# Kernel optimization log

Hardware: AMD Instinct MI355X
Metric: run time of the kernel (lower is better)

## Reference

```python
import jax, jax.numpy as jnp
import numpy as np

B, I, O, ORDER = 16384, 256, 256, 8
LO, HI = -1.0, 1.0


def setup_inputs() -> dict:
    key = jax.random.key(0)
    k1, k2, k3 = jax.random.split(key, 3)
    x = jax.random.normal(k1, (B, I), dtype=jnp.float32)
    weights = jax.random.normal(k2, (O, I), dtype=jnp.float32)
    # BernsteinBasisFunction init: randn(order+1) * 0.1, one per (o, i) pair
    coeffs = jax.random.normal(k3, (O, I, ORDER + 1), dtype=jnp.float32) * 0.1
    return {"x": x, "weights": weights, "coeffs": coeffs}


def reference(x, weights, coeffs):
    # x: [B, I]; weights: [O, I]; coeffs: [O, I, K+1]
    K = coeffs.shape[-1] - 1
    zoom = (HI - LO) / 2.0
    pan = (HI + LO) / 2.0
    xt = jnp.tanh(x) * zoom + pan          # squash into [LO, HI]
    x_a = xt - LO                          # [B, I]
    x_b = HI - xt                          # [B, I]
    e = jnp.arange(K + 1)
    # ber[b, i, k] = x_a^k * x_b^(K-k)  (unnormalized Bernstein basis)
    ber = (x_a[..., None] ** e) * (x_b[..., None] ** (K - e))  # [B, I, K+1]
    # transformed[b, o, i] = sum_k coeffs[o,i,k] * ber[b,i,k]; out = einsum('boi,oi->bo')
    # Fused: fold weights into coeffs to avoid the [B, O, I] intermediate.
    wc = coeffs * weights[..., None]       # [O, I, K+1]
    return jnp.einsum('bik,oik->bo', ber, wc)
```

## Files before the change

### kernel.cpp

```cpp
#include <hip/hip_runtime.h>
#include <hip/hip_bf16.h>


#define BDIM 16384
#define IDIM 256
#define ODIM 256
#define NK 9
#define NCHUNK 4
#define NSTEP 36
#define STEP_ELEMS (ODIM * 64)
#define CGW 4

typedef short short8 __attribute__((ext_vector_type(8)));
typedef float floatx4 __attribute__((ext_vector_type(4)));

__global__ __launch_bounds__(256) void prep_wc2(const float* __restrict__ weights,
                                                const float* __restrict__ coeffs,
                                                ushort* __restrict__ wc) {
    int idx  = blockIdx.x * 256 + threadIdx.x;
    int step = idx >> 11;
    int c    = idx & 2047;
    int big    = c >> 6;
    int lane_w = c & 63;
    int o    = (big >> 1) * 16 + (lane_w & 15);
    int s    = big & 1;
    int quad = lane_w >> 4;
    int ic = step / 9;
    int k  = step - ic * 9;
    int i0 = ic * 64 + s * 32 + quad * 8;

    const float* cp = coeffs + (size_t)(o * IDIM + i0) * NK + k;
    float4 w0 = *(const float4*)(weights + o * IDIM + i0);
    float4 w1 = *(const float4*)(weights + o * IDIM + i0 + 4);
    float wv[8] = {w0.x, w0.y, w0.z, w0.w, w1.x, w1.y, w1.z, w1.w};

    union { ushort us[8]; int4 v; __hip_bfloat162 h2[4]; } pk;
#pragma unroll
    for (int j = 0; j < 8; j += 2) {
        float a = cp[(size_t)j * NK] * wv[j];
        float b = cp[(size_t)(j + 1) * NK] * wv[j + 1];
        pk.h2[j >> 1] = __float22bfloat162_rn(make_float2(a, b));
    }
    *(int4*)(wc + (size_t)step * STEP_ELEMS + (size_t)c * 8) = pk.v;
}

__global__ __launch_bounds__(256, 2) void bern_gemm(const float* __restrict__ x,
                                                    const ushort* __restrict__ wc,
                                                    float* __restrict__ out) {
    __shared__ ushort Blds[2][16384];

    const int tid  = threadIdx.x;
    const int wave = tid >> 6;
    const int lane = tid & 63;
    const int cg   = blockIdx.x & 3;
    const int rb   = (blockIdx.x >> 2) * 128 + wave * 32;
    const int lrow = lane & 15;
    const int jseg = (lane >> 4) * 8;

    float p[2][2][8];
    float r[2][2][8];
    floatx4 acc[2][4];
    floatx4 zero = {0.0f, 0.0f, 0.0f, 0.0f};
#pragma unroll
    for (int m = 0; m < 2; ++m)
#pragma unroll
        for (int n = 0; n < 4; ++n)
            acc[m][n] = zero;

#define LOAD_XR(ic_)                                                            \
    {                                                                           \
        _Pragma("unroll") for (int m = 0; m < 2; ++m)                           \
        _Pragma("unroll") for (int s = 0; s < 2; ++s) {                         \
            const float* xp = x + (size_t)(rb + m * 16 + lrow) * IDIM           \
                              + (ic_) * 64 + s * 32 + jseg;                     \
            float4 v0 = *(const float4*)(xp);                                   \
            float4 v1 = *(const float4*)(xp + 4);                               \
            r[m][s][0] = v0.x; r[m][s][1] = v0.y;                               \
            r[m][s][2] = v0.z; r[m][s][3] = v0.w;                               \
            r[m][s][4] = v1.x; r[m][s][5] = v1.y;                               \
            r[m][s][6] = v1.z; r[m][s][7] = v1.w;                               \
        }                                                                       \
    }

#define SETUP_FROM_R()                                                          \
    {                                                                           \
        _Pragma("unroll") for (int m = 0; m < 2; ++m)                           \
        _Pragma("unroll") for (int s = 0; s < 2; ++s)                           \
        _Pragma("unroll") for (int e = 0; e < 8; ++e) {                         \
            float t  = __builtin_amdgcn_exp2f(r[m][s][e] * 2.8853900817779268f);\
            float q  = 2.0f * __builtin_amdgcn_rcpf(t + 1.0f);                  \
            float q2 = q * q;                                                   \
            float q4 = q2 * q2;                                                 \
            p[m][s][e] = q4 * q4;                                               \
            r[m][s][e] = t;                                                     \
        }                                                                       \
    }

#define STAGE(g_, b_)                                                           \
    {                                                                           \
        _Pragma("unroll") for (int q = 0; q < 4; ++q)                           \
        _Pragma("unroll") for (int h = 0; h < 2; ++h) {                         \
            int st  = (g_) * 4 + q;                                             \
            int off = wave * 1024 + h * 512 + lane * 8;                         \
            const ushort* sp = wc + (size_t)st * STEP_ELEMS + cg * 4096 + off;  \
            ushort* dp = &Blds[b_][q * 4096 + off];                             \
            __builtin_amdgcn_global_load_lds(                                   \
                (const __attribute__((address_space(1))) void*)sp,              \
                (__attribute__((address_space(3))) void*)dp, 16, 0, 0);         \
        }                                                                       \
    }

    LOAD_XR(0);
    SETUP_FROM_R();
    STAGE(0, 0);

#pragma unroll
    for (int g = 0; g < 9; ++g) {
        __syncthreads();
        if (g < 8) STAGE(g + 1, (g + 1) & 1);

#pragma unroll
        for (int k4 = 0; k4 < 4; ++k4) {
            const int step = g * 4 + k4;
            if (step == 8 || step == 17 || step == 26) {
                LOAD_XR(step / 9 + 1);
            }
            const int kin = step % 9;

#pragma unroll
            for (int s = 0; s < 2; ++s) {
                short8 bfr[4];
#pragma unroll
                for (int n = 0; n < 4; ++n)
                    bfr[n] = *(const short8*)&Blds[g & 1]
                        [k4 * 4096 + (n * 2 + s) * 512 + lane * 8];

#pragma unroll
                for (int m = 0; m < 2; ++m) {
                    union { ushort us[8]; short8 v; __hip_bfloat162 h2[4]; } pk;
#pragma unroll
                    for (int e = 0; e < 8; e += 2) {
                        pk.h2[e >> 1] = __float22bfloat162_rn(
                            make_float2(p[m][s][e], p[m][s][e + 1]));
                    }
#pragma unroll
                    for (int n = 0; n < 4; ++n)
                        acc[m][n] = __builtin_amdgcn_mfma_f32_16x16x32_bf16(
                            pk.v, bfr[n], acc[m][n], 0, 0, 0);
                    if (kin < NK - 1)
#pragma unroll
                        for (int e = 0; e < 8; ++e) p[m][s][e] *= r[m][s][e];
                }
            }

            if (step == 8 || step == 17 || step == 26) {
                SETUP_FROM_R();
            }
        }
    }

#pragma unroll
    for (int m = 0; m < 2; ++m) {
#pragma unroll
        for (int n = 0; n < 4; ++n) {
            int col   = cg * 64 + n * 16 + (lane & 15);
            int rbase = rb + m * 16 + (lane >> 4) * 4;
#pragma unroll
            for (int reg = 0; reg < 4; ++reg) {
                out[(size_t)(rbase + reg) * ODIM + col] = acc[m][n][reg];
            }
        }
    }
#undef LOAD_XR
#undef SETUP_FROM_R
#undef STAGE
}

extern "C" void kernel_launch(void* const* d_in, const int* in_sizes, int n_in,
                              void* d_out, int out_size, void* d_ws, size_t ws_size,
                              hipStream_t stream) {
    const float* x       = (const float*)d_in[0];
    const float* weights = (const float*)d_in[1];
    const float* coeffs  = (const float*)d_in[2];
    float* out = (float*)d_out;
    ushort* wc = (ushort*)d_ws;

    prep_wc2<<<288, 256, 0, stream>>>(weights, coeffs, wc);
    bern_gemm<<<512, 256, 0, stream>>>(x, wc, out);
}
```

Measured before the change: 98.48 us.

## Split K dimension across two wave groups with LDS reduction in bern_gemm

Doubles the block to 512 threads and splits the 36-step reduction over input chunks between two groups of four waves, each handling half the input chunks (18 steps). Each staging round now loads two steps per half into shared memory, and at the end one group writes partial accumulators to LDS for the other to add before storing. This raises the number of resident waves for latency hiding and halves the serial K loop per wave. The cost is an extra LDS reduction pass with two barriers, and the launch bound of four blocks of 512 threads puts pressure on the register budget.

```diff
diff --git a/kernel.cpp b/kernel.cpp
--- a/kernel.cpp
+++ b/kernel.cpp
@@ -6,10 +6,8 @@
 #define IDIM 256
 #define ODIM 256
 #define NK 9
-#define NCHUNK 4
 #define NSTEP 36
 #define STEP_ELEMS (ODIM * 64)
-#define CGW 4
 
 typedef short short8 __attribute__((ext_vector_type(8)));
 typedef float floatx4 __attribute__((ext_vector_type(4)));
@@ -44,7 +42,7 @@
     *(int4*)(wc + (size_t)step * STEP_ELEMS + (size_t)c * 8) = pk.v;
 }
 
-__global__ __launch_bounds__(256, 2) void bern_gemm(const float* __restrict__ x,
+__global__ __launch_bounds__(512, 4) void bern_gemm(const float* __restrict__ x,
                                                     const ushort* __restrict__ wc,
                                                     float* __restrict__ out) {
     __shared__ ushort Blds[2][16384];
@@ -52,8 +50,10 @@
     const int tid  = threadIdx.x;
     const int wave = tid >> 6;
     const int lane = tid & 63;
+    const int wl   = wave & 3;
+    const int wg   = wave >> 2;
     const int cg   = blockIdx.x & 3;
-    const int rb   = (blockIdx.x >> 2) * 128 + wave * 32;
+    const int rb   = (blockIdx.x >> 2) * 128 + wl * 32;
     const int lrow = lane & 15;
     const int jseg = (lane >> 4) * 8;
 
@@ -98,19 +98,19 @@
 
 #define STAGE(g_, b_)                                                           \
     {                                                                           \
-        _Pragma("unroll") for (int q = 0; q < 4; ++q)                           \
-        _Pragma("unroll") for (int h = 0; h < 2; ++h) {                         \
-            int st  = (g_) * 4 + q;                                             \
-            int off = wave * 1024 + h * 512 + lane * 8;                         \
+        _Pragma("unroll") for (int hq = 0; hq < 4; ++hq) {                      \
+            int half = hq >> 1, q = hq & 1;                                     \
+            int st  = half * 18 + (g_) * 2 + q;                                 \
+            int off = wave * 512 + lane * 8;                                    \
             const ushort* sp = wc + (size_t)st * STEP_ELEMS + cg * 4096 + off;  \
-            ushort* dp = &Blds[b_][q * 4096 + off];                             \
+            ushort* dp = &Blds[b_][(half * 2 + q) * 4096 + off];                \
             __builtin_amdgcn_global_load_lds(                                   \
                 (const __attribute__((address_space(1))) void*)sp,              \
                 (__attribute__((address_space(3))) void*)dp, 16, 0, 0);         \
         }                                                                       \
     }
 
-    LOAD_XR(0);
+    LOAD_XR(wg * 2);
     SETUP_FROM_R();
     STAGE(0, 0);
 
@@ -120,12 +120,10 @@
         if (g < 8) STAGE(g + 1, (g + 1) & 1);
 
 #pragma unroll
-        for (int k4 = 0; k4 < 4; ++k4) {
-            const int step = g * 4 + k4;
-            if (step == 8 || step == 17 || step == 26) {
-                LOAD_XR(step / 9 + 1);
-            }
-            const int kin = step % 9;
+        for (int q = 0; q < 2; ++q) {
+            const int t   = g * 2 + q;
+            const int kin = t % 9;
+            if (t == 8) LOAD_XR(wg * 2 + 1);
 
 #pragma unroll
             for (int s = 0; s < 2; ++s) {
@@ -133,7 +131,7 @@
 #pragma unroll
                 for (int n = 0; n < 4; ++n)
                     bfr[n] = *(const short8*)&Blds[g & 1]
-                        [k4 * 4096 + (n * 2 + s) * 512 + lane * 8];
+                        [(wg * 2 + q) * 4096 + (n * 2 + s) * 512 + lane * 8];
 
 #pragma unroll
                 for (int m = 0; m < 2; ++m) {
@@ -153,21 +151,35 @@
                 }
             }
 
-            if (step == 8 || step == 17 || step == 26) {
-                SETUP_FROM_R();
-            }
+            if (t == 8) SETUP_FROM_R();
         }
     }
 
-#pragma unroll
-    for (int m = 0; m < 2; ++m) {
-#pragma unroll
-        for (int n = 0; n < 4; ++n) {
-            int col   = cg * 64 + n * 16 + (lane & 15);
-            int rbase = rb + m * 16 + (lane >> 4) * 4;
-#pragma unroll
-            for (int reg = 0; reg < 4; ++reg) {
-                out[(size_t)(rbase + reg) * ODIM + col] = acc[m][n][reg];
+    __syncthreads();
+    float* fb = (float*)(&Blds[0][0]) + wl * 2048;
+    if (wg == 1) {
+#pragma unroll
+        for (int m = 0; m < 2; ++m)
+#pragma unroll
+            for (int n = 0; n < 4; ++n)
+#pragma unroll
+                for (int reg = 0; reg < 4; ++reg)
+                    fb[(((m * 4 + n) * 4) + reg) * 64 + lane] = acc[m][n][reg];
+    }
+    __syncthreads();
+    if (wg == 0) {
+#pragma unroll
+        for (int m = 0; m < 2; ++m) {
+#pragma unroll
+            for (int n = 0; n < 4; ++n) {
+                int col   = cg * 64 + n * 16 + (lane & 15);
+                int rbase = rb + m * 16 + (lane >> 4) * 4;
+#pragma unroll
+                for (int reg = 0; reg < 4; ++reg) {
+                    float v = acc[m][n][reg] +
+                              fb[(((m * 4 + n) * 4) + reg) * 64 + lane];
+                    out[(size_t)(rbase + reg) * ODIM + col] = v;
+                }
             }
         }
     }
@@ -186,5 +198,5 @@
     ushort* wc = (ushort*)d_ws;
 
     prep_wc2<<<288, 256, 0, stream>>>(weights, coeffs, wc);
-    bern_gemm<<<512, 256, 0, stream>>>(x, wc, out);
+    bern_gemm<<<512, 512, 0, stream>>>(x, wc, out);
 }
```

New measurement: 132.5 us. +34.6%, slower.
